# Performance work log

Measured on AMD Instinct MI355X. Metric: run time of the kernel, lower is better.

Reference implementation:

```python
import jax, jax.numpy as jnp
import numpy as np

E, N, D, H = 500000, 100000, 8, 256
BN_EPS = 1e-5


def _batchnorm(x, gamma, beta):
    # BatchNorm1d in training mode: biased batch statistics over dim 0
    mu = jnp.mean(x, axis=0)
    var = jnp.var(x, axis=0)
    return (x - mu) * jax.lax.rsqrt(var + BN_EPS) * gamma + beta


def _encoder(x, W1, b1, gamma, beta, W2, b2):
    h = jax.nn.relu(x @ W1 + b1)
    h = _batchnorm(h, gamma, beta)
    return h @ W2 + b2


def setup_inputs() -> dict:
    key = jax.random.key(0)
    ks = jax.random.split(key, 24)
    s = 0.05  # weight init scale
    inp = {
        "edge_attr": jax.random.normal(ks[0], (E, D), dtype=jnp.float32),
        "node_features": jax.random.normal(ks[1], (N, D), dtype=jnp.float32),
        "edge_index": jax.random.randint(ks[2], (2, E), 0, N, dtype=jnp.int32),
        "e_W1": jax.random.normal(ks[3], (D, H)) * s,
        "e_b1": jax.random.normal(ks[4], (H,)) * s,
        "e_gamma": jnp.ones((H,), jnp.float32),
        "e_beta": jnp.zeros((H,), jnp.float32),
        "e_W2": jax.random.normal(ks[5], (H, H)) * s,
        "e_b2": jax.random.normal(ks[6], (H,)) * s,
        "n_W1": jax.random.normal(ks[7], (D, H)) * s,
        "n_b1": jax.random.normal(ks[8], (H,)) * s,
        "n_gamma": jnp.ones((H,), jnp.float32),
        "n_beta": jnp.zeros((H,), jnp.float32),
        "n_W2": jax.random.normal(ks[9], (H, H)) * s,
        "n_b2": jax.random.normal(ks[10], (H,)) * s,
        "Wv": jax.random.normal(ks[11], (H, H)) * s,
        "bv": jax.random.normal(ks[12], (H,)) * s,
        "Wo": jax.random.normal(ks[13], (H, H)) * s,
        "bo": jax.random.normal(ks[14], (H,)) * s,
        "Wp": jax.random.normal(ks[15], (H, D)) * s,
        "bp": jax.random.normal(ks[16], (D,)) * s,
    }
    return inp


def reference(edge_attr, node_features, edge_index,
              e_W1, e_b1, e_gamma, e_beta, e_W2, e_b2,
              n_W1, n_b1, n_gamma, n_beta, n_W2, n_b2,
              Wv, bv, Wo, bo, Wp, bp):
    # edge encoder: Linear -> ReLU -> BatchNorm1d -> Linear
    edge_encoded = _encoder(edge_attr, e_W1, e_b1, e_gamma, e_beta, e_W2, e_b2)

    # gather endpoint features and average (node dim == edge dim, slice is no-op)
    src = node_features[edge_index[0]]  # [E, D]
    tgt = node_features[edge_index[1]]  # [E, D]
    node_context = (src + tgt) * 0.5
    node_encoded = _encoder(node_context, n_W1, n_b1, n_gamma, n_beta, n_W2, n_b2)

    # MultiheadAttention with seq_len=1: softmax over one key is exactly 1,
    # so output = out_proj(v_proj(node_encoded)); q/k projections cancel.
    attn_out = (node_encoded @ Wv + bv) @ Wo + bo  # [E, H]

    edge_attr_enhanced = attn_out @ Wp + bp  # [E, D]
    return edge_attr + 0.5 * edge_attr_enhanced
```

## Files before the change

### kernel.cpp

```cpp
#include <hip/hip_runtime.h>
#include <hip/hip_bf16.h>
#include <string.h>

#define E_CNT 500000
#define N_CNT 100000
#define HID   256
#define NTILE 31250

typedef short short8 __attribute__((ext_vector_type(8)));
typedef float f32x4 __attribute__((ext_vector_type(4)));

__device__ __forceinline__ unsigned short f2bf(float f){
  union { float f; unsigned int i; } v; v.f = f;
  unsigned int u = v.i;
  u = u + 0x7FFFu + ((u >> 16) & 1u);
  return (unsigned short)(u >> 16);
}

__device__ __forceinline__ unsigned int pk_bf16(float a, float b){
  __hip_bfloat162 p = __float22bfloat162_rn(make_float2(a, b));
  unsigned int u; memcpy(&u, &p, 4); return u;
}

__device__ __forceinline__ void init_w1_lds(unsigned short* w1l,
                                            const float* W1, const float* b1,
                                            int tid){
  int ch = tid;
  #pragma unroll
  for (int j = 0; j < 8; ++j){
    unsigned short w = f2bf(W1[j * HID + ch]);
    w1l[ch * 24 + j]     = w;
    w1l[ch * 24 + 8 + j] = w;
  }
  w1l[ch * 24 + 16] = f2bf(2.0f * b1[ch]);
  #pragma unroll
  for (int j = 17; j < 24; ++j) w1l[ch * 24 + j] = 0;
  if (tid < 32) w1l[256 * 24 + tid] = 0;
}

__global__ __launch_bounds__(256, 3) void k1_stats(
    const int* __restrict__ eidx, const float* __restrict__ nf,
    const float* __restrict__ W1, const float* __restrict__ b1,
    float* __restrict__ part, float* __restrict__ bd2,
    unsigned short* __restrict__ ctxw)
{
  __shared__ unsigned short w1l[256 * 24 + 32];
  __shared__ float sred[2][4][128];

  const int tid = threadIdx.x, lane = tid & 63, wid = tid >> 6;
  const int cg = wid & 1;
  const int pair = (blockIdx.x * 4 + wid) >> 1;
  const int npair = gridDim.x * 2;
  const int m = lane & 15, q = lane >> 4;

  if (blockIdx.x == 0 && tid < 16) bd2[tid] = 0.f;

  init_w1_lds(w1l, W1, b1, tid);
  __syncthreads();

  short8 w1fr[8];
  #pragma unroll
  for (int nt = 0; nt < 8; ++nt)
    w1fr[nt] = *(const short8*)&w1l[((cg * 8 + nt) * 16 + m) * 24 + q * 8];

  const f32x4 z4 = {0.f, 0.f, 0.f, 0.f};
  f32x4 sacc[8], qacc[8];
  #pragma unroll
  for (int nt = 0; nt < 8; ++nt){ sacc[nt] = z4; qacc[nt] = z4; }

  short8 kc = {0,0,0,0,0,0,0,0};
  if (q == 2) kc[0] = (short)0x3F80;
  const bool ld = (q < 2);

  int t = pair;
  int idc = 0;
  float4 nfa = make_float4(0.f,0.f,0.f,0.f), nfb = nfa;
  if (ld){
    int id0 = eidx[q * E_CNT + t * 16 + m];
    nfa = ((const float4*)nf)[id0 * 2];
    nfb = ((const float4*)nf)[id0 * 2 + 1];
    int tn = t + npair;
    if (tn < NTILE) idc = eidx[q * E_CNT + tn * 16 + m];
  }

  for (; t < NTILE; t += npair){
    short8 bfr = kc;
    if (ld){
      union { short8 s; uint4 u; } bu;
      bu.u = make_uint4(pk_bf16(nfa.x, nfa.y), pk_bf16(nfa.z, nfa.w),
                        pk_bf16(nfb.x, nfb.y), pk_bf16(nfb.z, nfb.w));
      bfr = bu.s;
      if (cg == 0)
        *(uint4*)&ctxw[(size_t)t * 256 + q * 128 + m * 8] = bu.u;
    }

    int tn1 = t + npair, tn2 = t + 2 * npair;
    if (ld && tn1 < NTILE){
      nfa = ((const float4*)nf)[idc * 2];
      nfb = ((const float4*)nf)[idc * 2 + 1];
      if (tn2 < NTILE) idc = eidx[q * E_CNT + tn2 * 16 + m];
    }

    #pragma unroll
    for (int nt = 0; nt < 8; ++nt){
      f32x4 c = __builtin_amdgcn_mfma_f32_16x16x32_bf16(w1fr[nt], bfr, z4, 0, 0, 0);
      f32x4 hv = __builtin_elementwise_max(c, z4);
      sacc[nt] += hv;
      qacc[nt] += hv * hv;
    }
  }

  #pragma unroll
  for (int nt = 0; nt < 8; ++nt){
    #pragma unroll
    for (int i = 0; i < 4; ++i){
      float v = sacc[nt][i], w = qacc[nt][i];
      v += __shfl_xor(v, 1); w += __shfl_xor(w, 1);
      v += __shfl_xor(v, 2); w += __shfl_xor(w, 2);
      v += __shfl_xor(v, 4); w += __shfl_xor(w, 4);
      v += __shfl_xor(v, 8); w += __shfl_xor(w, 8);
      if (m == 0){
        int loc = nt * 16 + q * 4 + i;
        sred[0][wid][loc] = v;
        sred[1][wid][loc] = w;
      }
    }
  }
  __syncthreads();
  {
    int j = tid, hf = j >> 7, loc = j & 127;
    float s0 = sred[0][hf][loc] + sred[0][hf + 2][loc];
    float s1 = sred[1][hf][loc] + sred[1][hf + 2][loc];
    part[blockIdx.x * 512 + j]       = s0;
    part[blockIdx.x * 512 + 256 + j] = s1;
  }
}

__global__ __launch_bounds__(256) void kMid(
    const float* __restrict__ part, int nb,
    const float* __restrict__ gamma, const float* __restrict__ beta,
    const float* __restrict__ nW2,
    const float* __restrict__ Wv, const float* __restrict__ Wo,
    const float* __restrict__ Wp,
    const float* __restrict__ bv, const float* __restrict__ bo,
    const float* __restrict__ bp, const float* __restrict__ nb2,
    unsigned short* __restrict__ wd2t, float* __restrict__ bd2)
{
  __shared__ float WpL[2048];
  __shared__ float T1L[2048];
  __shared__ float T2L[2048];
  __shared__ float scr[2048];
  __shared__ float stL[8];
  const int t = threadIdx.x, b = blockIdx.x;

  for (int i = t; i < 2048; i += 256) WpL[i] = Wp[i];
  __syncthreads();

  {
    const float4* row = (const float4*)(Wo + t * HID);
    f32x4 a0 = {0.f,0.f,0.f,0.f}, a1 = {0.f,0.f,0.f,0.f};
    #pragma unroll 8
    for (int j4 = 0; j4 < 64; ++j4){
      float4 w = row[j4];
      const f32x4* xp = (const f32x4*)&WpL[j4 * 32];
      a0 += w.x * xp[0]; a1 += w.x * xp[1];
      a0 += w.y * xp[2]; a1 += w.y * xp[3];
      a0 += w.z * xp[4]; a1 += w.z * xp[5];
      a0 += w.w * xp[6]; a1 += w.w * xp[7];
    }
    *(f32x4*)&T1L[t * 8]     = a0;
    *(f32x4*)&T1L[t * 8 + 4] = a1;
  }
  __syncthreads();

  {
    const float4* row = (const float4*)(Wv + t * HID);
    f32x4 a0 = {0.f,0.f,0.f,0.f}, a1 = {0.f,0.f,0.f,0.f};
    #pragma unroll 8
    for (int j4 = 0; j4 < 64; ++j4){
      float4 w = row[j4];
      const f32x4* xp = (const f32x4*)&T1L[j4 * 32];
      a0 += w.x * xp[0]; a1 += w.x * xp[1];
      a0 += w.y * xp[2]; a1 += w.y * xp[3];
      a0 += w.z * xp[4]; a1 += w.z * xp[5];
      a0 += w.w * xp[6]; a1 += w.w * xp[7];
    }
    *(f32x4*)&T2L[t * 8]     = a0;
    *(f32x4*)&T2L[t * 8 + 4] = a1;
  }
  __syncthreads();

  {
    int cl = t >> 6, i = t & 63;
    int c = b * 4 + cl;
    float s0 = 0.f, s1 = 0.f;
    for (int b2 = i; b2 < nb; b2 += 64){
      s0 += part[b2 * 512 + c];
      s1 += part[b2 * 512 + 256 + c];
    }
    scr[cl * 128 + i]      = s0;
    scr[cl * 128 + 64 + i] = s1;
  }
  __syncthreads();
  if (t < 4){
    float s0 = 0.f, s1 = 0.f;
    for (int i = 0; i < 64; ++i){
      s0 += scr[t * 128 + i];
      s1 += scr[t * 128 + 64 + i];
    }
    const float invE = 1.0f / (float)E_CNT;
    float mu  = s0 * invE;
    float var = fmaxf(s1 * invE - mu * mu, 0.f);
    float s   = gamma[b * 4 + t] * rsqrtf(var + 4.0f * 1e-5f);
    stL[t]     = s;
    stL[4 + t] = beta[b * 4 + t] - mu * s;
  }
  __syncthreads();

  {
    int cl = t >> 6, d = (t >> 3) & 7, p8 = t & 7;
    int c = b * 4 + cl;
    const float* row = nW2 + c * HID;
    float a = 0.f;
    for (int j = p8 * 32; j < p8 * 32 + 32; ++j)
      a = fmaf(row[j], T2L[j * 8 + d], a);
    scr[t] = a;
  }
  __syncthreads();
  {
    int cl = t >> 6, d = (t >> 3) & 7, p8 = t & 7;
    if (p8 == 0){
      float w = 0.f;
      #pragma unroll
      for (int i = 0; i < 8; ++i) w += scr[t + i];
      int c = b * 4 + cl;
      wd2t[d * HID + c]       = f2bf(0.5f * stL[cl] * w);
      wd2t[(8 + d) * HID + c] = 0;
      scr[1024 + cl * 8 + d]  = stL[4 + cl] * w;
    }
  }
  __syncthreads();
  if (t < 8){
    float a = scr[1024 + t] + scr[1024 + 8 + t] +
              scr[1024 + 16 + t] + scr[1024 + 24 + t];
    #pragma unroll
    for (int jj = 0; jj < 4; ++jj){
      int j = 4 * b + jj;
      a = fmaf(nb2[j], T2L[j * 8 + t], a);
      a = fmaf(bv[j],  T1L[j * 8 + t], a);
      a = fmaf(bo[j],  WpL[j * 8 + t], a);
    }
    if (b == 0) a += bp[t];
    atomicAdd(&bd2[t], a);
  }
}

__global__ __launch_bounds__(256, 3) void k3_main(
    const float* __restrict__ ea,
    const float* __restrict__ W1, const float* __restrict__ b1,
    const unsigned short* __restrict__ wd2t, const float* __restrict__ bd2,
    const unsigned short* __restrict__ ctxw,
    float* __restrict__ out)
{
  __shared__ __align__(16) unsigned short smem[4 * 16 * 264];

  const int tid = threadIdx.x, lane = tid & 63, wid = tid >> 6;
  const int gw = blockIdx.x * 4 + wid, ngw = gridDim.x * 4;
  const int m = lane & 15, q = lane >> 4;

  init_w1_lds(smem, W1, b1, tid);

  short8 w2fr[8];
  #pragma unroll
  for (int kb = 0; kb < 8; ++kb)
    w2fr[kb] = *(const short8*)&wd2t[m * HID + kb * 32 + q * 8];
  const float bd2v = (m < 8) ? 0.5f * bd2[m] : 0.f;

  __syncthreads();

  short8 w1fr[16];
  #pragma unroll
  for (int nt = 0; nt < 16; ++nt)
    w1fr[nt] = *(const short8*)&smem[(nt * 16 + m) * 24 + q * 8];

  __syncthreads();
  unsigned short* myh = smem + wid * (16 * 264);

  const f32x4 z4 = {0.f, 0.f, 0.f, 0.f};

  short8 kc = {0,0,0,0,0,0,0,0};
  if (q == 2) kc[0] = (short)0x3F80;
  const bool ld  = (q < 2);
  const bool dok = (m < 8);

  int t = gw;
  short8 bcur = kc;
  if (ld && t < NTILE)
    bcur = *(const short8*)&ctxw[(size_t)t * 256 + q * 128 + m * 8];

  for (; t < NTILE; t += ngw){
    int tn = t + ngw;
    short8 bnext = kc;
    if (ld && tn < NTILE)
      bnext = *(const short8*)&ctxw[(size_t)tn * 256 + q * 128 + m * 8];

    float eav[4];
    #pragma unroll
    for (int i = 0; i < 4; ++i)
      eav[i] = dok ? ea[(t * 16 + q * 4 + i) * 8 + m] : 0.f;

    #pragma unroll
    for (int nt = 0; nt < 16; ++nt){
      f32x4 c = __builtin_amdgcn_mfma_f32_16x16x32_bf16(w1fr[nt], bcur, z4, 0, 0, 0);
      f32x4 hv = __builtin_elementwise_max(c, z4);
      *(uint2*)&myh[m * 264 + nt * 16 + q * 4] =
          make_uint2(pk_bf16(hv[0], hv[1]), pk_bf16(hv[2], hv[3]));
    }
    asm volatile("s_waitcnt lgkmcnt(0)" ::: "memory");
    f32x4 acc0 = z4, acc1 = z4;
    #pragma unroll
    for (int kb = 0; kb < 4; ++kb){
      short8 a0 = *(const short8*)&myh[m * 264 + (2*kb)   * 32 + q * 8];
      short8 a1 = *(const short8*)&myh[m * 264 + (2*kb+1) * 32 + q * 8];
      acc0 = __builtin_amdgcn_mfma_f32_16x16x32_bf16(a0, w2fr[2*kb],   acc0, 0, 0, 0);
      acc1 = __builtin_amdgcn_mfma_f32_16x16x32_bf16(a1, w2fr[2*kb+1], acc1, 0, 0, 0);
    }
    if (dok){
      #pragma unroll
      for (int i = 0; i < 4; ++i){
        float o = eav[i] + acc0[i] + acc1[i] + bd2v;
        out[(t * 16 + q * 4 + i) * 8 + m] = o;
      }
    }
    bcur = bnext;
  }
}

extern "C" void kernel_launch(void* const* d_in, const int* in_sizes, int n_in,
                              void* d_out, int out_size, void* d_ws, size_t ws_size,
                              hipStream_t stream)
{
  const float* ea   = (const float*)d_in[0];
  const float* nf   = (const float*)d_in[1];
  const int*   eidx = (const int*)d_in[2];
  const float* nW1    = (const float*)d_in[9];
  const float* nb1    = (const float*)d_in[10];
  const float* ngamma = (const float*)d_in[11];
  const float* nbeta  = (const float*)d_in[12];
  const float* nW2    = (const float*)d_in[13];
  const float* nb2    = (const float*)d_in[14];
  const float* Wv     = (const float*)d_in[15];
  const float* bv     = (const float*)d_in[16];
  const float* Wo     = (const float*)d_in[17];
  const float* bo     = (const float*)d_in[18];
  const float* Wp     = (const float*)d_in[19];
  const float* bp     = (const float*)d_in[20];

  const size_t CTX_BYTES = (size_t)NTILE * 512;
  long avail = (long)ws_size - 8192 - 64 - (long)CTX_BYTES - 1024;
  int nb = (int)(avail / 2048);
  if (nb > 1024) nb = 1024;
  if (nb < 1)    nb = 1;

  char* ws = (char*)d_ws;
  size_t off = (size_t)nb * 2048;
  float* ws_part          = (float*)(ws + 0);
  unsigned short* ws_wd2t = (unsigned short*)(ws + off);
  float* ws_bd2           = (float*)(ws + off + 8192);
  unsigned short* ws_ctx  = (unsigned short*)(ws + off + 8192 + 64);

  k1_stats<<<dim3(nb), dim3(256), 0, stream>>>(eidx, nf, nW1, nb1,
                                               ws_part, ws_bd2, ws_ctx);
  kMid<<<dim3(64), dim3(256), 0, stream>>>(
      ws_part, nb, ngamma, nbeta, nW2, Wv, Wo, Wp, bv, bo, bp, nb2,
      ws_wd2t, ws_bd2);
  k3_main<<<dim3(1024), dim3(256), 0, stream>>>(
      ea, nW1, nb1, ws_wd2t, ws_bd2, ws_ctx, (float*)d_out);
}
```

Before: 197.6 us.

## Fuse three kernels into one cooperative kernel with grid-wide syncs

Replaces the stats, weight-folding and main kernels with a single cooperative kernel that uses grid.sync() between phases. The W1 weights stay in LDS across phases and launch gaps are removed. The grid size is taken from an occupancy query and capped at 768 blocks, with a fallback to the old three-kernel path. The risks are grid-sync overhead, lower occupancy from the larger shared pool, and fewer blocks in the streaming phases. The workspace layout is also changed to a fixed 1024-block partial-sum region.

```diff
diff --git a/kernel.cpp b/kernel.cpp
--- a/kernel.cpp
+++ b/kernel.cpp
@@ -1,6 +1,9 @@
 #include <hip/hip_runtime.h>
 #include <hip/hip_bf16.h>
+#include <hip/hip_cooperative_groups.h>
 #include <string.h>
+
+namespace cg = cooperative_groups;
 
 #define E_CNT 500000
 #define N_CNT 100000
@@ -36,6 +39,297 @@
   #pragma unroll
   for (int j = 17; j < 24; ++j) w1l[ch * 24 + j] = 0;
   if (tid < 32) w1l[256 * 24 + tid] = 0;
+}
+
+__global__ __launch_bounds__(256) void kFused(
+    const int* __restrict__ eidx, const float* __restrict__ nf,
+    const float* __restrict__ ea,
+    const float* __restrict__ W1, const float* __restrict__ b1,
+    const float* __restrict__ gamma, const float* __restrict__ beta,
+    const float* __restrict__ nW2,
+    const float* __restrict__ Wv, const float* __restrict__ Wo,
+    const float* __restrict__ Wp,
+    const float* __restrict__ bv, const float* __restrict__ bo,
+    const float* __restrict__ bp, const float* __restrict__ nb2,
+    float* __restrict__ part, unsigned short* __restrict__ wd2t,
+    float* __restrict__ bd2, unsigned short* __restrict__ ctxw,
+    float* __restrict__ out)
+{
+  __shared__ unsigned short w1l[256 * 24 + 32];
+  __shared__ __align__(16) unsigned char pool[33824];
+
+  const int tid = threadIdx.x, lane = tid & 63, wid = tid >> 6;
+  const int m = lane & 15, q = lane >> 4;
+  const f32x4 z4 = {0.f, 0.f, 0.f, 0.f};
+
+  {
+    float* sred = (float*)pool;
+    const int cg = wid & 1;
+    const int pair = (blockIdx.x * 4 + wid) >> 1;
+    const int npair = gridDim.x * 2;
+
+    if (blockIdx.x == 0 && tid < 16) bd2[tid] = 0.f;
+
+    init_w1_lds(w1l, W1, b1, tid);
+    __syncthreads();
+
+    short8 w1fr[8];
+    #pragma unroll
+    for (int nt = 0; nt < 8; ++nt)
+      w1fr[nt] = *(const short8*)&w1l[((cg * 8 + nt) * 16 + m) * 24 + q * 8];
+
+    f32x4 sacc[8], qacc[8];
+    #pragma unroll
+    for (int nt = 0; nt < 8; ++nt){ sacc[nt] = z4; qacc[nt] = z4; }
+
+    short8 kc = {0,0,0,0,0,0,0,0};
+    if (q == 2) kc[0] = (short)0x3F80;
+    const bool ld = (q < 2);
+
+    int t = pair;
+    int idc = 0;
+    float4 nfa = make_float4(0.f,0.f,0.f,0.f), nfb = nfa;
+    if (ld){
+      int id0 = eidx[q * E_CNT + t * 16 + m];
+      nfa = ((const float4*)nf)[id0 * 2];
+      nfb = ((const float4*)nf)[id0 * 2 + 1];
+      int tn = t + npair;
+      if (tn < NTILE) idc = eidx[q * E_CNT + tn * 16 + m];
+    }
+
+    for (; t < NTILE; t += npair){
+      short8 bfr = kc;
+      if (ld){
+        union { short8 s; uint4 u; } bu;
+        bu.u = make_uint4(pk_bf16(nfa.x, nfa.y), pk_bf16(nfa.z, nfa.w),
+                          pk_bf16(nfb.x, nfb.y), pk_bf16(nfb.z, nfb.w));
+        bfr = bu.s;
+        if (cg == 0)
+          *(uint4*)&ctxw[(size_t)t * 256 + q * 128 + m * 8] = bu.u;
+      }
+
+      int tn1 = t + npair, tn2 = t + 2 * npair;
+      if (ld && tn1 < NTILE){
+        nfa = ((const float4*)nf)[idc * 2];
+        nfb = ((const float4*)nf)[idc * 2 + 1];
+        if (tn2 < NTILE) idc = eidx[q * E_CNT + tn2 * 16 + m];
+      }
+
+      #pragma unroll
+      for (int nt = 0; nt < 8; ++nt){
+        f32x4 c = __builtin_amdgcn_mfma_f32_16x16x32_bf16(w1fr[nt], bfr, z4, 0, 0, 0);
+        f32x4 hv = __builtin_elementwise_max(c, z4);
+        sacc[nt] += hv;
+        qacc[nt] += hv * hv;
+      }
+    }
+
+    #pragma unroll
+    for (int nt = 0; nt < 8; ++nt){
+      #pragma unroll
+      for (int i = 0; i < 4; ++i){
+        float v = sacc[nt][i], w = qacc[nt][i];
+        v += __shfl_xor(v, 1); w += __shfl_xor(w, 1);
+        v += __shfl_xor(v, 2); w += __shfl_xor(w, 2);
+        v += __shfl_xor(v, 4); w += __shfl_xor(w, 4);
+        v += __shfl_xor(v, 8); w += __shfl_xor(w, 8);
+        if (m == 0){
+          int loc = nt * 16 + q * 4 + i;
+          sred[(0 * 4 + wid) * 128 + loc] = v;
+          sred[(1 * 4 + wid) * 128 + loc] = w;
+        }
+      }
+    }
+    __syncthreads();
+    {
+      int j = tid, hf = j >> 7, loc = j & 127;
+      float s0 = sred[(0*4 + hf) * 128 + loc] + sred[(0*4 + hf + 2) * 128 + loc];
+      float s1 = sred[(1*4 + hf) * 128 + loc] + sred[(1*4 + hf + 2) * 128 + loc];
+      part[blockIdx.x * 512 + j]       = s0;
+      part[blockIdx.x * 512 + 256 + j] = s1;
+    }
+  }
+
+  cg::this_grid().sync();
+
+  if (blockIdx.x < 64){
+    float* WpL = (float*)pool;
+    float* T1L = WpL + 2048;
+    float* T2L = T1L + 2048;
+    float* scr = T2L + 2048;
+    float* stL = scr + 2048;
+    const int t = tid, b = blockIdx.x;
+    const int nb = (int)gridDim.x;
+
+    for (int i = t; i < 2048; i += 256) WpL[i] = Wp[i];
+    __syncthreads();
+
+    {
+      const float4* row = (const float4*)(Wo + t * HID);
+      f32x4 a0 = z4, a1 = z4;
+      #pragma unroll 8
+      for (int j4 = 0; j4 < 64; ++j4){
+        float4 w = row[j4];
+        const f32x4* xp = (const f32x4*)&WpL[j4 * 32];
+        a0 += w.x * xp[0]; a1 += w.x * xp[1];
+        a0 += w.y * xp[2]; a1 += w.y * xp[3];
+        a0 += w.z * xp[4]; a1 += w.z * xp[5];
+        a0 += w.w * xp[6]; a1 += w.w * xp[7];
+      }
+      *(f32x4*)&T1L[t * 8]     = a0;
+      *(f32x4*)&T1L[t * 8 + 4] = a1;
+    }
+    __syncthreads();
+
+    {
+      const float4* row = (const float4*)(Wv + t * HID);
+      f32x4 a0 = z4, a1 = z4;
+      #pragma unroll 8
+      for (int j4 = 0; j4 < 64; ++j4){
+        float4 w = row[j4];
+        const f32x4* xp = (const f32x4*)&T1L[j4 * 32];
+        a0 += w.x * xp[0]; a1 += w.x * xp[1];
+        a0 += w.y * xp[2]; a1 += w.y * xp[3];
+        a0 += w.z * xp[4]; a1 += w.z * xp[5];
+        a0 += w.w * xp[6]; a1 += w.w * xp[7];
+      }
+      *(f32x4*)&T2L[t * 8]     = a0;
+      *(f32x4*)&T2L[t * 8 + 4] = a1;
+    }
+    __syncthreads();
+
+    {
+      int cl = t >> 6, i = t & 63;
+      int c = b * 4 + cl;
+      float s0 = 0.f, s1 = 0.f;
+      for (int b2 = i; b2 < nb; b2 += 64){
+        s0 += part[b2 * 512 + c];
+        s1 += part[b2 * 512 + 256 + c];
+      }
+      scr[cl * 128 + i]      = s0;
+      scr[cl * 128 + 64 + i] = s1;
+    }
+    __syncthreads();
+    if (t < 4){
+      float s0 = 0.f, s1 = 0.f;
+      for (int i = 0; i < 64; ++i){
+        s0 += scr[t * 128 + i];
+        s1 += scr[t * 128 + 64 + i];
+      }
+      const float invE = 1.0f / (float)E_CNT;
+      float mu  = s0 * invE;
+      float var = fmaxf(s1 * invE - mu * mu, 0.f);
+      float s   = gamma[b * 4 + t] * rsqrtf(var + 4.0f * 1e-5f);
+      stL[t]     = s;
+      stL[4 + t] = beta[b * 4 + t] - mu * s;
+    }
+    __syncthreads();
+
+    {
+      int cl = t >> 6, d = (t >> 3) & 7, p8 = t & 7;
+      int c = b * 4 + cl;
+      const float* row = nW2 + c * HID;
+      float a = 0.f;
+      for (int j = p8 * 32; j < p8 * 32 + 32; ++j)
+        a = fmaf(row[j], T2L[j * 8 + d], a);
+      __syncthreads();
+      scr[t] = a;
+    }
+    __syncthreads();
+    {
+      int cl = t >> 6, d = (t >> 3) & 7, p8 = t & 7;
+      if (p8 == 0){
+        float w = 0.f;
+        #pragma unroll
+        for (int i = 0; i < 8; ++i) w += scr[t + i];
+        int c = b * 4 + cl;
+        wd2t[d * HID + c]       = f2bf(0.5f * stL[cl] * w);
+        wd2t[(8 + d) * HID + c] = 0;
+        scr[1024 + cl * 8 + d]  = stL[4 + cl] * w;
+      }
+    }
+    __syncthreads();
+    if (t < 8){
+      float a = scr[1024 + t] + scr[1024 + 8 + t] +
+                scr[1024 + 16 + t] + scr[1024 + 24 + t];
+      #pragma unroll
+      for (int jj = 0; jj < 4; ++jj){
+        int j = 4 * b + jj;
+        a = fmaf(nb2[j], T2L[j * 8 + t], a);
+        a = fmaf(bv[j],  T1L[j * 8 + t], a);
+        a = fmaf(bo[j],  WpL[j * 8 + t], a);
+      }
+      if (b == 0) a += bp[t];
+      atomicAdd(&bd2[t], a);
+    }
+  }
+
+  cg::this_grid().sync();
+
+  {
+    unsigned short* hb = (unsigned short*)pool;
+    const int gw = blockIdx.x * 4 + wid, ngw = gridDim.x * 4;
+
+    short8 w2fr[8];
+    #pragma unroll
+    for (int kb = 0; kb < 8; ++kb)
+      w2fr[kb] = *(const short8*)&wd2t[m * HID + kb * 32 + q * 8];
+    const float bd2v = (m < 8) ? 0.5f * bd2[m] : 0.f;
+
+    short8 w1fr[16];
+    #pragma unroll
+    for (int nt = 0; nt < 16; ++nt)
+      w1fr[nt] = *(const short8*)&w1l[(nt * 16 + m) * 24 + q * 8];
+
+    unsigned short* myh = hb + wid * (16 * 264);
+
+    short8 kc = {0,0,0,0,0,0,0,0};
+    if (q == 2) kc[0] = (short)0x3F80;
+    const bool ld  = (q < 2);
+    const bool dok = (m < 8);
+
+    int t = gw;
+    short8 bcur = kc;
+    if (ld && t < NTILE)
+      bcur = *(const short8*)&ctxw[(size_t)t * 256 + q * 128 + m * 8];
+
+    for (; t < NTILE; t += ngw){
+      int tn = t + ngw;
+      short8 bnext = kc;
+      if (ld && tn < NTILE)
+        bnext = *(const short8*)&ctxw[(size_t)tn * 256 + q * 128 + m * 8];
+
+      float eav[4];
+      #pragma unroll
+      for (int i = 0; i < 4; ++i)
+        eav[i] = dok ? ea[(t * 16 + q * 4 + i) * 8 + m] : 0.f;
+
+      #pragma unroll
+      for (int nt = 0; nt < 16; ++nt){
+        f32x4 c = __builtin_amdgcn_mfma_f32_16x16x32_bf16(w1fr[nt], bcur, z4, 0, 0, 0);
+        f32x4 hv = __builtin_elementwise_max(c, z4);
+        *(uint2*)&myh[m * 264 + nt * 16 + q * 4] =
+            make_uint2(pk_bf16(hv[0], hv[1]), pk_bf16(hv[2], hv[3]));
+      }
+      asm volatile("s_waitcnt lgkmcnt(0)" ::: "memory");
+      f32x4 acc0 = z4, acc1 = z4;
+      #pragma unroll
+      for (int kb = 0; kb < 4; ++kb){
+        short8 a0 = *(const short8*)&myh[m * 264 + (2*kb)   * 32 + q * 8];
+        short8 a1 = *(const short8*)&myh[m * 264 + (2*kb+1) * 32 + q * 8];
+        acc0 = __builtin_amdgcn_mfma_f32_16x16x32_bf16(a0, w2fr[2*kb],   acc0, 0, 0, 0);
+        acc1 = __builtin_amdgcn_mfma_f32_16x16x32_bf16(a1, w2fr[2*kb+1], acc1, 0, 0, 0);
+      }
+      if (dok){
+        #pragma unroll
+        for (int i = 0; i < 4; ++i){
+          float o = eav[i] + acc0[i] + acc1[i] + bd2v;
+          out[(t * 16 + q * 4 + i) * 8 + m] = o;
+        }
+      }
+      bcur = bnext;
+    }
+  }
 }
 
 __global__ __launch_bounds__(256, 3) void k1_stats(
@@ -356,24 +650,39 @@
   const float* Wp     = (const float*)d_in[19];
   const float* bp     = (const float*)d_in[20];
 
-  const size_t CTX_BYTES = (size_t)NTILE * 512;
-  long avail = (long)ws_size - 8192 - 64 - (long)CTX_BYTES - 1024;
-  int nb = (int)(avail / 2048);
-  if (nb > 1024) nb = 1024;
-  if (nb < 1)    nb = 1;
-
   char* ws = (char*)d_ws;
-  size_t off = (size_t)nb * 2048;
+  const size_t PART_BYTES = (size_t)1024 * 2048;
   float* ws_part          = (float*)(ws + 0);
-  unsigned short* ws_wd2t = (unsigned short*)(ws + off);
-  float* ws_bd2           = (float*)(ws + off + 8192);
-  unsigned short* ws_ctx  = (unsigned short*)(ws + off + 8192 + 64);
-
+  unsigned short* ws_wd2t = (unsigned short*)(ws + PART_BYTES);
+  float* ws_bd2           = (float*)(ws + PART_BYTES + 8192);
+  unsigned short* ws_ctx  = (unsigned short*)(ws + PART_BYTES + 8192 + 64);
+  float* outp = (float*)d_out;
+
+  int maxB = 0;
+  hipError_t qe = hipOccupancyMaxActiveBlocksPerMultiprocessor(&maxB, kFused, 256, 0);
+  int grid = (qe == hipSuccess) ? maxB * 256 : 0;
+  if (grid > 768) grid = 768;
+
+  if (grid >= 64){
+    void* args[] = {
+      (void*)&eidx, (void*)&nf, (void*)&ea, (void*)&nW1, (void*)&nb1,
+      (void*)&ngamma, (void*)&nbeta, (void*)&nW2,
+      (void*)&Wv, (void*)&Wo, (void*)&Wp,
+      (void*)&bv, (void*)&bo, (void*)&bp, (void*)&nb2,
+      (void*)&ws_part, (void*)&ws_wd2t, (void*)&ws_bd2, (void*)&ws_ctx,
+      (void*)&outp
+    };
+    hipError_t le = hipLaunchCooperativeKernel(kFused, dim3(grid), dim3(256),
+                                               args, 0, stream);
+    if (le == hipSuccess) return;
+  }
+
+  int nb = 1024;
   k1_stats<<<dim3(nb), dim3(256), 0, stream>>>(eidx, nf, nW1, nb1,
                                                ws_part, ws_bd2, ws_ctx);
   kMid<<<dim3(64), dim3(256), 0, stream>>>(
       ws_part, nb, ngamma, nbeta, nW2, Wv, Wo, Wp, bv, bo, bp, nb2,
       ws_wd2t, ws_bd2);
   k3_main<<<dim3(1024), dim3(256), 0, stream>>>(
-      ea, nW1, nb1, ws_wd2t, ws_bd2, ws_ctx, (float*)d_out);
-}
+      ea, nW1, nb1, ws_wd2t, ws_bd2, ws_ctx, outp);
+}
```

New measurement: 313.7 us. 58.7% more time.
